# Optimization experiments

Hardware: AMD Instinct MI355X
Metric: run time of the kernel (lower is better)

The kernel has to match this reference:

```python
import jax, jax.numpy as jnp
import numpy as np
from jax import lax

WIN = 7
PAD = WIN // 2
K1, K2 = 0.01, 0.03
NP = WIN * WIN
COV_NORM = NP / (NP - 1)  # use_sample_covariance=True


def _dwconv(x, w, channel):
    # depthwise 2D conv, SAME-style explicit padding (torch conv2d padding=pad)
    return lax.conv_general_dilated(
        x, w, window_strides=(1, 1),
        padding=[(PAD, PAD), (PAD, PAD)],
        feature_group_count=channel,
        dimension_numbers=('NCHW', 'OIHW', 'NCHW'))


def setup_inputs() -> dict:
    key = jax.random.key(0)
    k1, k2 = jax.random.split(key)
    B, C, H, W = 64, 1, 384, 384
    gt = jax.random.uniform(k1, (B, C, H, W), dtype=jnp.float32)
    pred = jax.random.uniform(k2, (B, C, H, W), dtype=jnp.float32)
    # uniform (box) window: create_window(7, channel=1, gaussian_weights=False)
    window = jnp.ones((C, 1, WIN, WIN), dtype=jnp.float32) / NP
    return {"gt": gt, "pred": pred, "window": window}


def reference(gt, pred, window):
    channel = gt.shape[1]
    data_range = jnp.max(gt)  # data_range=None default

    ux = _dwconv(gt, window, channel)
    uy = _dwconv(pred, window, channel)
    uxx = _dwconv(gt * gt, window, channel) - ux * ux
    uyy = _dwconv(pred * pred, window, channel) - uy * uy
    uxy = _dwconv(gt * pred, window, channel) - ux * uy

    vx = COV_NORM * uxx
    vy = COV_NORM * uyy
    vxy = COV_NORM * uxy

    C1 = (K1 * data_range) ** 2
    C2 = (K2 * data_range) ** 2

    S = (2.0 * ux * uy + C1) * (2.0 * vxy + C2) / ((ux * ux + uy * uy + C1) * (vx + vy + C2))
    ssim_map = S[:, :, PAD:-PAD, PAD:-PAD]
    return jnp.mean(ssim_map)  # size_average=True, full=False
```

## Files before the change

### kernel.cpp

```cpp
#include <hip/hip_runtime.h>


#define PADW 3
#define BT 64
#define BAND 15
#define SROWS (BAND + 6)

constexpr int B_ = 64, H_ = 384, W_ = 384;
constexpr int W2 = W_ / 2;
constexpr int OUTD = W_ - 2 * PADW;
constexpr int NBANDS = (OUTD + BAND - 1) / BAND;
constexpr int NTILES = 3;
constexpr int TOTAL_BLOCKS = NTILES * NBANDS * B_;
constexpr double NPIX = (double)B_ * OUTD * OUTD;

__device__ __forceinline__ unsigned enc_f(float f) {
    unsigned u = __float_as_uint(f);
    return (u & 0x80000000u) ? ~u : (u | 0x80000000u);
}
__device__ __forceinline__ float dec_f(unsigned e) {
    return __uint_as_float((e & 0x80000000u) ? (e & 0x7fffffffu) : ~e);
}

__device__ __forceinline__ float2 f2add(float2 a, float2 b) { return make_float2(a.x + b.x, a.y + b.y); }
__device__ __forceinline__ float2 f2sub(float2 a, float2 b) { return make_float2(a.x - b.x, a.y - b.y); }

__device__ __forceinline__ void glds16(const void* g, void* l) {
    __builtin_amdgcn_global_load_lds(
        (const __attribute__((address_space(1))) void*)g,
        (__attribute__((address_space(3))) void*)l, 16, 0, 0);
}

__global__ void __launch_bounds__(256)
max_kernel(const float4* __restrict__ g4, unsigned* ws_max, int n4) {
    int tid = blockIdx.x * blockDim.x + threadIdx.x;
    int stride = gridDim.x * blockDim.x;
    float m = -3.402823466e38f;
    for (int i = tid; i < n4; i += stride) {
        float4 v = g4[i];
        m = fmaxf(m, fmaxf(fmaxf(v.x, v.y), fmaxf(v.z, v.w)));
    }
#pragma unroll
    for (int off = 32; off > 0; off >>= 1)
        m = fmaxf(m, __shfl_down(m, off));
    __shared__ float sm[4];
    if ((threadIdx.x & 63) == 0) sm[threadIdx.x >> 6] = m;
    __syncthreads();
    if (threadIdx.x == 0) {
        float mm = fmaxf(fmaxf(sm[0], sm[1]), fmaxf(sm[2], sm[3]));
        atomicMax(ws_max, enc_f(mm));
    }
}

__device__ __forceinline__ float ssim_px(float sx, float sy, float sxx, float syy, float sxy,
                                         float C1, float C2) {
    const float inv49 = 1.0f / 49.0f;
    const float covn  = 49.0f / 48.0f;
    float ux  = sx * inv49, uy = sy * inv49;
    float uxx = sxx * inv49 - ux * ux;
    float uyy = syy * inv49 - uy * uy;
    float uxy = sxy * inv49 - ux * uy;
    float vvx = covn * uxx, vvy = covn * uyy, vvxy = covn * uxy;
    float num = (2.0f * ux * uy + C1) * (2.0f * vvxy + C2);
    float den = (ux * ux + uy * uy + C1) * (vvx + vvy + C2);
    return num / den;
}

__global__ void __launch_bounds__(BT)
ssim_kernel(const float* __restrict__ gt, const float* __restrict__ pred,
            const unsigned* __restrict__ ws_max, double* __restrict__ ws_part) {
    const int t    = threadIdx.x;
    const int tile = blockIdx.x;
    const int band = blockIdx.y;
    const int b    = blockIdx.z;
    const int bid  = (b * NBANDS + band) * NTILES + tile;

    const int  row0   = band * BAND;
    const int  cbase2 = tile * 63;
    const int  base2  = cbase2 & ~1;
    const int  off    = cbase2 & 1;
    const int  maxoff = W_ * 4 - base2 * 8 - 16;
    const bool active = (t < 63);

    __shared__ __align__(16) float2 sg[SROWS][68], sp[SROWS][68];

    const float2* gbase = (const float2*)(gt   + (size_t)b * H_ * W_);
    const float2* pbase = (const float2*)(pred + (size_t)b * H_ * W_);

    const int laneoff = min(t * 16, maxoff);

    if (t < 34) {
#pragma unroll
        for (int r = 0; r < SROWS; ++r) {
            const int ir = min(row0 + r, H_ - 1);
            const char* grb = (const char*)(gbase + (size_t)ir * W2 + base2);
            const char* prb = (const char*)(pbase + (size_t)ir * W2 + base2);
            glds16(grb + laneoff, &sg[r][0]);
            glds16(prb + laneoff, &sp[r][0]);
        }
    }

    const float dr = dec_f(*ws_max);
    const float C1 = (0.01f * dr) * (0.01f * dr);
    const float C2 = (0.03f * dr) * (0.03f * dr);

    float2 rx[7], ry[7], rxx[7], ryy[7], rxy[7];
#pragma unroll
    for (int j = 0; j < 7; ++j) {
        rx[j] = make_float2(0.f, 0.f); ry[j] = rx[j];
        rxx[j] = rx[j]; ryy[j] = rx[j]; rxy[j] = rx[j];
    }
    float2 vx = make_float2(0.f, 0.f), vy = vx, vxx = vx, vyy = vx, vxy = vx;
    double acc = 0.0;

#pragma unroll 1
    for (int g = 0; g < 3; ++g) {
#pragma unroll
        for (int j = 0; j < 7; ++j) {
            const int i  = g * 7 + j;
            const int ti = t + off;
            const float2* rg = sg[i];
            const float2* rp = sp[i];
            float2 d0 = rg[ti], d1 = rg[ti + 1], d2 = rg[ti + 2], d3 = rg[ti + 3];
            float2 e0 = rp[ti], e1 = rp[ti + 1], e2 = rp[ti + 2], e3 = rp[ti + 3];

            float hx0 = d0.x + d0.y + d1.x + d1.y + d2.x + d2.y + d3.x;
            float hy0 = e0.x + e0.y + e1.x + e1.y + e2.x + e2.y + e3.x;
            float hxx0 = fmaf(d0.x, d0.x, fmaf(d0.y, d0.y, fmaf(d1.x, d1.x,
                         fmaf(d1.y, d1.y, fmaf(d2.x, d2.x, fmaf(d2.y, d2.y, d3.x * d3.x))))));
            float hyy0 = fmaf(e0.x, e0.x, fmaf(e0.y, e0.y, fmaf(e1.x, e1.x,
                         fmaf(e1.y, e1.y, fmaf(e2.x, e2.x, fmaf(e2.y, e2.y, e3.x * e3.x))))));
            float hxy0 = fmaf(d0.x, e0.x, fmaf(d0.y, e0.y, fmaf(d1.x, e1.x,
                         fmaf(d1.y, e1.y, fmaf(d2.x, e2.x, fmaf(d2.y, e2.y, d3.x * e3.x))))));

            float2 h_x  = make_float2(hx0,  hx0  - d0.x        + d3.y);
            float2 h_y  = make_float2(hy0,  hy0  - e0.x        + e3.y);
            float2 h_xx = make_float2(hxx0, hxx0 - d0.x * d0.x + d3.y * d3.y);
            float2 h_yy = make_float2(hyy0, hyy0 - e0.x * e0.x + e3.y * e3.y);
            float2 h_xy = make_float2(hxy0, hxy0 - d0.x * e0.x + d3.y * e3.y);

            vx  = f2add(vx,  f2sub(h_x,  rx[j]));  rx[j]  = h_x;
            vy  = f2add(vy,  f2sub(h_y,  ry[j]));  ry[j]  = h_y;
            vxx = f2add(vxx, f2sub(h_xx, rxx[j])); rxx[j] = h_xx;
            vyy = f2add(vyy, f2sub(h_yy, ryy[j])); ryy[j] = h_yy;
            vxy = f2add(vxy, f2sub(h_xy, rxy[j])); rxy[j] = h_xy;

            const int orow = row0 + i - 6;
            if (i >= 6 && active && orow < OUTD) {
                acc += (double)ssim_px(vx.x, vy.x, vxx.x, vyy.x, vxy.x, C1, C2)
                     + (double)ssim_px(vx.y, vy.y, vxx.y, vyy.y, vxy.y, C1, C2);
            }
        }
    }

#pragma unroll
    for (int off2 = 32; off2 > 0; off2 >>= 1)
        acc += __shfl_down(acc, off2);
    if (t == 0) ws_part[bid] = acc;
}

__global__ void __launch_bounds__(256)
final_kernel(const double* __restrict__ ws_part, float* __restrict__ out) {
    const int t = threadIdx.x;
    double s = 0.0;
    for (int i = t; i < TOTAL_BLOCKS; i += 256) s += ws_part[i];
#pragma unroll
    for (int off = 32; off > 0; off >>= 1)
        s += __shfl_down(s, off);
    __shared__ double sd[4];
    if ((t & 63) == 0) sd[t >> 6] = s;
    __syncthreads();
    if (t == 0) out[0] = (float)((sd[0] + sd[1] + sd[2] + sd[3]) / NPIX);
}

extern "C" void kernel_launch(void* const* d_in, const int* in_sizes, int n_in,
                              void* d_out, int out_size, void* d_ws, size_t ws_size,
                              hipStream_t stream) {
    const float* gt   = (const float*)d_in[0];
    const float* pred = (const float*)d_in[1];
    float* out = (float*)d_out;

    unsigned* ws_max  = (unsigned*)d_ws;
    double*   ws_part = (double*)((char*)d_ws + 64);


    const int n4 = B_ * H_ * W_ / 4;
    max_kernel<<<1024, 256, 0, stream>>>((const float4*)gt, ws_max, n4);

    dim3 grid(NTILES, NBANDS, B_);
    ssim_kernel<<<grid, BT, 0, stream>>>(gt, pred, ws_max, ws_part);

    final_kernel<<<1, 256, 0, stream>>>(ws_part, out);
}
```

Before: 145.1 us.

## Load input rows directly from global memory and simplify SSIM pixel algebra

Drops the LDS staging, which used async global_load_lds of 21 rows into shared memory. Each thread now reads its four float2 values per row straight from global memory, relying on L1/L2 to serve the overlapping neighbour reads. The per-pixel SSIM formula is also rewritten to work on raw window sums with constants scaled by 49^2, which removes several multiplies. This removes the LDS round trip and the wait on the staging, but it issues many more overlapping global loads per thread and loses the bulk prefetch of all rows up front.

```diff
diff --git a/kernel.cpp b/kernel.cpp
--- a/kernel.cpp
+++ b/kernel.cpp
@@ -25,12 +25,6 @@
 __device__ __forceinline__ float2 f2add(float2 a, float2 b) { return make_float2(a.x + b.x, a.y + b.y); }
 __device__ __forceinline__ float2 f2sub(float2 a, float2 b) { return make_float2(a.x - b.x, a.y - b.y); }
 
-__device__ __forceinline__ void glds16(const void* g, void* l) {
-    __builtin_amdgcn_global_load_lds(
-        (const __attribute__((address_space(1))) void*)g,
-        (__attribute__((address_space(3))) void*)l, 16, 0, 0);
-}
-
 __global__ void __launch_bounds__(256)
 max_kernel(const float4* __restrict__ g4, unsigned* ws_max, int n4) {
     int tid = blockIdx.x * blockDim.x + threadIdx.x;
@@ -52,18 +46,20 @@
     }
 }
 
-__device__ __forceinline__ float ssim_px(float sx, float sy, float sxx, float syy, float sxy,
-                                         float C1, float C2) {
-    const float inv49 = 1.0f / 49.0f;
-    const float covn  = 49.0f / 48.0f;
-    float ux  = sx * inv49, uy = sy * inv49;
-    float uxx = sxx * inv49 - ux * ux;
-    float uyy = syy * inv49 - uy * uy;
-    float uxy = sxy * inv49 - ux * uy;
-    float vvx = covn * uxx, vvy = covn * uyy, vvxy = covn * uxy;
-    float num = (2.0f * ux * uy + C1) * (2.0f * vvxy + C2);
-    float den = (ux * ux + uy * uy + C1) * (vvx + vvy + C2);
-    return num / den;
+__device__ __forceinline__ float ssim_px(float a, float b, float sxx, float syy, float sxy,
+                                         float C1q, float C2q) {
+    const float covn = 49.0f / 48.0f;
+    float ab   = a * b;
+    float num1 = fmaf(2.0f, ab, C1q);
+    float txy  = fmaf(49.0f, sxy, -ab);
+    float num2 = fmaf(2.0f * covn, txy, C2q);
+    float b2   = b * b;
+    float aabb = fmaf(a, a, b2);
+    float den1 = aabb + C1q;
+    float spq  = sxx + syy;
+    float tv   = fmaf(49.0f, spq, -aabb);
+    float den2 = fmaf(covn, tv, C2q);
+    return (num1 * num2) / (den1 * den2);
 }
 
 __global__ void __launch_bounds__(BT)
@@ -75,34 +71,18 @@
     const int b    = blockIdx.z;
     const int bid  = (b * NBANDS + band) * NTILES + tile;
 
+    const float dr  = dec_f(*ws_max);
+    const float c1  = 0.01f * dr, c2 = 0.03f * dr;
+    const float C1q = c1 * c1 * 2401.0f;
+    const float C2q = c2 * c2 * 2401.0f;
+
     const int  row0   = band * BAND;
-    const int  cbase2 = tile * 63;
-    const int  base2  = cbase2 & ~1;
-    const int  off    = cbase2 & 1;
-    const int  maxoff = W_ * 4 - base2 * 8 - 16;
     const bool active = (t < 63);
 
-    __shared__ __align__(16) float2 sg[SROWS][68], sp[SROWS][68];
+    const int tb = min(tile * 63 + t, W2 - 4);
 
-    const float2* gbase = (const float2*)(gt   + (size_t)b * H_ * W_);
-    const float2* pbase = (const float2*)(pred + (size_t)b * H_ * W_);
-
-    const int laneoff = min(t * 16, maxoff);
-
-    if (t < 34) {
-#pragma unroll
-        for (int r = 0; r < SROWS; ++r) {
-            const int ir = min(row0 + r, H_ - 1);
-            const char* grb = (const char*)(gbase + (size_t)ir * W2 + base2);
-            const char* prb = (const char*)(pbase + (size_t)ir * W2 + base2);
-            glds16(grb + laneoff, &sg[r][0]);
-            glds16(prb + laneoff, &sp[r][0]);
-        }
-    }
-
-    const float dr = dec_f(*ws_max);
-    const float C1 = (0.01f * dr) * (0.01f * dr);
-    const float C2 = (0.03f * dr) * (0.03f * dr);
+    const float2* gp = (const float2*)(gt   + (size_t)b * H_ * W_) + tb;
+    const float2* pp = (const float2*)(pred + (size_t)b * H_ * W_) + tb;
 
     float2 rx[7], ry[7], rxx[7], ryy[7], rxy[7];
 #pragma unroll
@@ -118,11 +98,11 @@
 #pragma unroll
         for (int j = 0; j < 7; ++j) {
             const int i  = g * 7 + j;
-            const int ti = t + off;
-            const float2* rg = sg[i];
-            const float2* rp = sp[i];
-            float2 d0 = rg[ti], d1 = rg[ti + 1], d2 = rg[ti + 2], d3 = rg[ti + 3];
-            float2 e0 = rp[ti], e1 = rp[ti + 1], e2 = rp[ti + 2], e3 = rp[ti + 3];
+            const int ir = min(row0 + i, H_ - 1);
+            const float2* gr = gp + (size_t)ir * W2;
+            const float2* pr = pp + (size_t)ir * W2;
+            float2 d0 = gr[0], d1 = gr[1], d2 = gr[2], d3 = gr[3];
+            float2 e0 = pr[0], e1 = pr[1], e2 = pr[2], e3 = pr[3];
 
             float hx0 = d0.x + d0.y + d1.x + d1.y + d2.x + d2.y + d3.x;
             float hy0 = e0.x + e0.y + e1.x + e1.y + e2.x + e2.y + e3.x;
@@ -147,8 +127,8 @@
 
             const int orow = row0 + i - 6;
             if (i >= 6 && active && orow < OUTD) {
-                acc += (double)ssim_px(vx.x, vy.x, vxx.x, vyy.x, vxy.x, C1, C2)
-                     + (double)ssim_px(vx.y, vy.y, vxx.y, vyy.y, vxy.y, C1, C2);
+                acc += (double)ssim_px(vx.x, vy.x, vxx.x, vyy.x, vxy.x, C1q, C2q)
+                     + (double)ssim_px(vx.y, vy.y, vxx.y, vyy.y, vxy.y, C1q, C2q);
             }
         }
     }
```

Result: faster. 141.1 us (-2.8%).
